# Performance work log

Hardware: AMD Instinct MI355X
Metric: run time of the kernel (lower is better)

The kernel has to match this reference:

```python
import jax, jax.numpy as jnp
import numpy as np
import math

B, S, H, N = 1, 4096, 1024, 16
HN = H // N  # 64

def setup_inputs() -> dict:
    key = jax.random.key(0)
    k1, k2, k3 = jax.random.split(key, 3)
    hidden_states = jax.random.normal(k1, (B, S, H), dtype=jnp.float32)
    # lower-triangular causal mask, float {0,1}, broadcastable to [b,np,s,s]
    ltor_mask = jnp.tril(jnp.ones((1, 1, S, S), dtype=jnp.float32))
    w_qkv = jax.random.normal(k2, (3 * H, H), dtype=jnp.float32) * 0.02
    b_qkv = jnp.zeros((3 * H,), dtype=jnp.float32)
    w_dense = jax.random.normal(k3, (H, H), dtype=jnp.float32) * 0.02
    b_dense = jnp.zeros((H,), dtype=jnp.float32)
    return {"hidden_states": hidden_states, "ltor_mask": ltor_mask,
            "w_qkv": w_qkv, "b_qkv": b_qkv,
            "w_dense": w_dense, "b_dense": b_dense}

def reference(hidden_states, ltor_mask, w_qkv, b_qkv, w_dense, b_dense):
    b, s, h = hidden_states.shape
    # fused QKV projection: [b,s,3h]
    mixed = jnp.einsum('bsh,oh->bso', hidden_states, w_qkv) + b_qkv
    q, k, v = jnp.split(mixed, 3, axis=-1)
    # [b,s,h] -> [b,n,s,hn]
    def heads(t):
        return t.reshape(b, s, N, HN).transpose(0, 2, 1, 3)
    q, k, v = heads(q), heads(k), heads(v)
    # raw scores [b,n,s,s]
    scores = jnp.einsum('bnqd,bnkd->bnqk', q, k) / math.sqrt(HN)
    # multiplicative mask plus -10000 additive for masked positions
    scores = scores * ltor_mask - 10000.0 * (1.0 - ltor_mask)
    probs = jax.nn.softmax(scores, axis=-1)
    # attention dropout prob = 0.0 -> identity
    ctx = jnp.einsum('bnqk,bnkd->bnqd', probs, v)
    ctx = ctx.transpose(0, 2, 1, 3).reshape(b, s, h)
    out = jnp.einsum('bsh,oh->bso', ctx, w_dense) + b_dense
    # output dropout prob = 0.0 -> identity
    return out
```

## Files before the change

kernel.cpp:

```cpp
#include <hip/hip_runtime.h>
#include <hip/hip_bf16.h>

static constexpr int SEQ  = 4096;
static constexpr int HID  = 1024;
static constexpr int NHEAD = 16;
static constexpr int HDIM  = 64;
static constexpr int H3   = 3072;

typedef __attribute__((ext_vector_type(8))) __bf16 bf16x8;
typedef __attribute__((ext_vector_type(4))) float  f32x4;

__device__ __forceinline__ float bf2f(unsigned short u) {
    union { unsigned int u; float f; } v; v.u = ((unsigned int)u) << 16; return v.f;
}
__device__ __forceinline__ unsigned short f2bf(float f) {
    union { float f; unsigned int u; } v; v.f = f;
    unsigned int r = v.u + 0x7fffu + ((v.u >> 16) & 1u);
    return (unsigned short)(r >> 16);
}
__device__ __forceinline__ void gl_lds16(const unsigned short* g, unsigned short* l) {
    __builtin_amdgcn_global_load_lds(
        (const __attribute__((address_space(1))) void*)g,
        (__attribute__((address_space(3))) void*)l, 16, 0, 0);
}

struct Conv5 { const float* src[5]; unsigned short* dst[5]; };

__global__ __launch_bounds__(256) void convert5(Conv5 c) {
    constexpr int cnt[5]  = {4194304, 3145728, 3072, 1048576, 1024};
    constexpr int boff[5] = {0, 2048, 3584, 3586, 4098};
    const int b = blockIdx.x;
    int t = 0, rel = b;
#pragma unroll
    for (int k = 1; k < 5; ++k) if (b >= boff[k]) { t = k; rel = b - boff[k]; }
    const int base = rel * 2048 + threadIdx.x * 8;
    if (base >= cnt[t]) return;
    const float* s = c.src[t] + base;
    const float4 a = ((const float4*)s)[0];
    const float4 b2 = ((const float4*)s)[1];
    union { unsigned short v[8]; uint4 q; } u;
    u.v[0] = f2bf(a.x); u.v[1] = f2bf(a.y); u.v[2] = f2bf(a.z); u.v[3] = f2bf(a.w);
    u.v[4] = f2bf(b2.x); u.v[5] = f2bf(b2.y); u.v[6] = f2bf(b2.z); u.v[7] = f2bf(b2.w);
    *(uint4*)(c.dst[t] + base) = u.q;
}

template <int BM, int BN, int BK, typename OutT, bool VFUSE>
__global__ __launch_bounds__(256) void gemm_bt(
    const unsigned short* __restrict__ A, const unsigned short* __restrict__ B,
    const unsigned short* __restrict__ bias, OutT* __restrict__ C,
    unsigned short* __restrict__ vt,
    int M, int N, int K)
{
    constexpr int MI  = BM / 32;
    constexpr int NI  = BN / 32;
    constexpr int KC  = BK / 32;
    constexpr int CB  = BK / 8;
    constexpr int LSH = (BK == 32) ? 2 : 3;
    constexpr int RPC = 64 >> LSH;

    const int tid  = threadIdx.x;
    const int wave = tid >> 6, lane = tid & 63;
    const int quad = lane >> 4, c16 = lane & 15;
    const int m0 = blockIdx.y * BM, n0 = blockIdx.x * BN;
    const int wr = wave >> 1, wc = wave & 1;

    __shared__ __align__(16) unsigned short sA[BM * BK];
    __shared__ __align__(16) unsigned short sB[BN * BK];

    f32x4 acc[MI][NI];
#pragma unroll
    for (int i = 0; i < MI; ++i)
#pragma unroll
        for (int j = 0; j < NI; ++j) acc[i][j] = {0.f, 0.f, 0.f, 0.f};

    const int sr = lane >> LSH;
    const int sc = ((lane & (CB - 1)) ^ (sr & (CB - 1))) * 8;

    for (int k0 = 0; k0 < K; k0 += BK) {
#pragma unroll
        for (int cc = 0; cc < BM / RPC / 4; ++cc) {
            const int rbase = cc * (4 * RPC) + wave * RPC;
            gl_lds16(A + (size_t)(m0 + rbase + sr) * K + k0 + sc, &sA[rbase * BK]);
        }
#pragma unroll
        for (int cc = 0; cc < BN / RPC / 4; ++cc) {
            const int rbase = cc * (4 * RPC) + wave * RPC;
            gl_lds16(B + (size_t)(n0 + rbase + sr) * K + k0 + sc, &sB[rbase * BK]);
        }
        __syncthreads();

#pragma unroll
        for (int kc = 0; kc < KC; ++kc) {
            bf16x8 af[MI], bfr[NI];
#pragma unroll
            for (int i = 0; i < MI; ++i) {
                const int ra = wr * (BM / 2) + i * 16 + c16;
                af[i] = *(const bf16x8*)&sA[ra * BK + (((kc * 4 + quad) ^ ra) & (CB - 1)) * 8];
            }
#pragma unroll
            for (int j = 0; j < NI; ++j) {
                const int rb = wc * (BN / 2) + j * 16 + c16;
                bfr[j] = *(const bf16x8*)&sB[rb * BK + (((kc * 4 + quad) ^ rb) & (CB - 1)) * 8];
            }
#pragma unroll
            for (int i = 0; i < MI; ++i)
#pragma unroll
                for (int j = 0; j < NI; ++j)
                    acc[i][j] = __builtin_amdgcn_mfma_f32_16x16x32_bf16(af[i], bfr[j], acc[i][j], 0, 0, 0);
        }
        __syncthreads();
    }

    if constexpr (VFUSE) {
        if (n0 >= 2048) {
#pragma unroll
            for (int j = 0; j < NI; ++j) {
                const int col = n0 + wc * (BN / 2) + j * 16 + c16;
                const float bv = bf2f(bias[col]);
                const int d  = col - 2048;
                unsigned short* vrow = vt + (size_t)d * SEQ;
#pragma unroll
                for (int i = 0; i < MI; ++i) {
                    const int base32 = m0 + wr * (BM / 2) + (i >> 1) * 32;
                    const int phys = base32 + 8 * quad + 4 * (i & 1);
                    union { unsigned short u[4]; uint2 q2; } w;
#pragma unroll
                    for (int r = 0; r < 4; ++r) w.u[r] = f2bf(acc[i][j][r] + bv);
                    *(uint2*)&vrow[phys] = w.q2;
                }
            }
            return;
        }
    }

#pragma unroll
    for (int j = 0; j < NI; ++j) {
        const int col = n0 + wc * (BN / 2) + j * 16 + c16;
        const float bv = bf2f(bias[col]);
#pragma unroll
        for (int i = 0; i < MI; ++i) {
#pragma unroll
            for (int r = 0; r < 4; ++r) {
                const int row = m0 + wr * (BM / 2) + i * 16 + quad * 4 + r;
                const float v = acc[i][j][r] + bv;
                if constexpr (sizeof(OutT) == 2) C[(size_t)row * N + col] = (OutT)f2bf(v);
                else                             C[(size_t)row * N + col] = (OutT)v;
            }
        }
    }
}

__global__ __launch_bounds__(256) void attn_causal(
    const unsigned short* __restrict__ qkv, const unsigned short* __restrict__ vt,
    unsigned short* __restrict__ ctx)
{
    const int bx = blockIdx.x;
    const int n  = bx & 15;
    const int p  = bx >> 4;
    const int tid  = threadIdx.x;
    const int wave = tid >> 6, lane = tid & 63;
    const int quad = lane >> 4, c16 = lane & 15;
    const int qg  = wave & 1;
    const int kvh = wave >> 1;

    __shared__ __align__(16) unsigned short smem[16384];
    unsigned short* smem_k = smem;
    unsigned short* smem_v = smem + 8192;

    const float QS = 0.125f * 1.44269504f;
    const int srow8 = lane >> 3;
    const int scol8 = ((lane & 7) ^ (lane >> 3)) * 8;
    const int srow4 = lane >> 4;

#pragma unroll 1
    for (int t = 0; t < 2; ++t) {
        const int z = t ? p : 63 - p;
        const int qrow0 = z * 64 + qg * 32;

        bf16x8 qf[2][2];
#pragma unroll
        for (int wq = 0; wq < 2; ++wq)
#pragma unroll
            for (int kc = 0; kc < 2; ++kc) {
                bf16x8 q = *(const bf16x8*)(qkv + (size_t)(qrow0 + wq * 16 + c16) * H3 + n * HDIM + kc * 32 + quad * 8);
#pragma unroll
                for (int j = 0; j < 8; ++j) q[j] = (__bf16)((float)q[j] * QS);
                qf[wq][kc] = q;
            }

        f32x4 o[2][4];
#pragma unroll
        for (int wq = 0; wq < 2; ++wq)
#pragma unroll
            for (int dt = 0; dt < 4; ++dt) o[wq][dt] = {0.f, 0.f, 0.f, 0.f};
        float l_i[2] = {0.f, 0.f};

        const int nkb = (z + 2) >> 1;
        for (int kb = 0; kb < nkb; ++kb) {
            const int kv0 = kb * 128;
#pragma unroll
            for (int cc = 0; cc < 4; ++cc) {
                const int rb = wave * 32 + cc * 8;
                gl_lds16(qkv + (size_t)(kv0 + rb + srow8) * H3 + HID + n * HDIM + scol8,
                         &smem_k[rb * 64]);
            }
#pragma unroll
            for (int cc = 0; cc < 4; ++cc) {
                const int rb = wave * 16 + cc * 4;
                const int sv = (((lane & 15) ^ ((cc * 4 + srow4) & 15))) * 8;
                gl_lds16(vt + (size_t)(n * HDIM + rb + srow4) * SEQ + kv0 + sv,
                         &smem_v[rb * 128]);
            }
            __syncthreads();

            const int kv0w = kv0 + kvh * 64;
            if (kv0w <= qrow0 + 31) {
                f32x4 s[2][4];
#pragma unroll
                for (int wq = 0; wq < 2; ++wq)
#pragma unroll
                    for (int mt = 0; mt < 4; ++mt) s[wq][mt] = {0.f, 0.f, 0.f, 0.f};
#pragma unroll
                for (int mt = 0; mt < 4; ++mt) {
                    const int krow = kvh * 64 + mt * 16 + c16;
                    const bf16x8 kf0 = *(const bf16x8*)&smem_k[krow * 64 + ((quad)     ^ (krow & 7)) * 8];
                    const bf16x8 kf1 = *(const bf16x8*)&smem_k[krow * 64 + ((4 + quad) ^ (krow & 7)) * 8];
#pragma unroll
                    for (int wq = 0; wq < 2; ++wq) {
                        s[wq][mt] = __builtin_amdgcn_mfma_f32_16x16x32_bf16(kf0, qf[wq][0], s[wq][mt], 0, 0, 0);
                        s[wq][mt] = __builtin_amdgcn_mfma_f32_16x16x32_bf16(kf1, qf[wq][1], s[wq][mt], 0, 0, 0);
                    }
                }

#pragma unroll
                for (int wq = 0; wq < 2; ++wq) {
                    if (kv0w + 63 > qrow0 + wq * 16) {
                        const int q_g = qrow0 + wq * 16 + c16;
#pragma unroll
                        for (int mt = 0; mt < 4; ++mt)
#pragma unroll
                            for (int r = 0; r < 4; ++r) {
                                const int kv = kv0w + mt * 16 + quad * 4 + r;
                                if (kv > q_g) s[wq][mt][r] = -30000.0f;
                            }
                    }
                    float rs = 0.f;
#pragma unroll
                    for (int mt = 0; mt < 4; ++mt)
#pragma unroll
                        for (int r = 0; r < 4; ++r) {
                            const float pp = __builtin_amdgcn_exp2f(s[wq][mt][r]);
                            s[wq][mt][r] = pp;
                            rs += pp;
                        }
                    l_i[wq] += rs;
                }

                bf16x8 pf[2][2];
#pragma unroll
                for (int wq = 0; wq < 2; ++wq)
#pragma unroll
                    for (int kc = 0; kc < 2; ++kc) {
                        union { __bf16 b[8]; bf16x8 v; } pp;
#pragma unroll
                        for (int r = 0; r < 4; ++r) {
                            pp.b[r]     = (__bf16)s[wq][2 * kc][r];
                            pp.b[4 + r] = (__bf16)s[wq][2 * kc + 1][r];
                        }
                        pf[wq][kc] = pp.v;
                    }

#pragma unroll
                for (int kc = 0; kc < 2; ++kc) {
#pragma unroll
                    for (int dt = 0; dt < 4; ++dt) {
                        const int vrow = dt * 16 + c16;
                        const int pc8 = (kvh * 8 + kc * 4 + quad) ^ (vrow & 15);
                        const bf16x8 vf = *(const bf16x8*)&smem_v[vrow * 128 + pc8 * 8];
#pragma unroll
                        for (int wq = 0; wq < 2; ++wq)
                            o[wq][dt] = __builtin_amdgcn_mfma_f32_16x16x32_bf16(vf, pf[wq][kc], o[wq][dt], 0, 0, 0);
                    }
                }
            }
            __syncthreads();
        }

#pragma unroll
        for (int wq = 0; wq < 2; ++wq) {
            l_i[wq] += __shfl_xor(l_i[wq], 16);
            l_i[wq] += __shfl_xor(l_i[wq], 32);
        }

        float* cb = (float*)smem;
        float* lb = (float*)(smem + 8704);
        unsigned short* fb = smem + 8832;

        if (kvh == 0) {
#pragma unroll
            for (int wq = 0; wq < 2; ++wq) {
#pragma unroll
                for (int dt = 0; dt < 4; ++dt)
                    *(f32x4*)&cb[(qg * 32 + wq * 16 + c16) * 68 + dt * 16 + quad * 4] = o[wq][dt];
                if (quad == 0) lb[qg * 32 + wq * 16 + c16] = l_i[wq];
            }
        }
        __syncthreads();
        if (kvh == 1) {
#pragma unroll
            for (int wq = 0; wq < 2; ++wq) {
                const float inv = 1.0f / (l_i[wq] + lb[qg * 32 + wq * 16 + c16]);
#pragma unroll
                for (int dt = 0; dt < 4; ++dt) {
                    const f32x4 pv = *(const f32x4*)&cb[(qg * 32 + wq * 16 + c16) * 68 + dt * 16 + quad * 4];
                    union { unsigned short u[4]; uint2 q2; } w;
#pragma unroll
                    for (int r = 0; r < 4; ++r) w.u[r] = f2bf((o[wq][dt][r] + pv[r]) * inv);
                    *(uint2*)&fb[(qg * 32 + wq * 16 + c16) * 72 + dt * 16 + quad * 4] = w.q2;
                }
            }
        }
        __syncthreads();

        const int qr = tid >> 2;
        const int xc = (tid & 3) * 16;
        unsigned short* dst = ctx + (size_t)(z * 64 + qr) * HID + n * HDIM + xc;
        *(uint4*)dst       = *(const uint4*)&fb[qr * 72 + xc];
        *(uint4*)(dst + 8) = *(const uint4*)&fb[qr * 72 + xc + 8];

        __syncthreads();
    }
}

extern "C" void kernel_launch(void* const* d_in, const int* in_sizes, int n_in,
                              void* d_out, int out_size, void* d_ws, size_t ws_size,
                              hipStream_t stream)
{
    unsigned short* base = (unsigned short*)d_ws;

    unsigned short* hs_c = base;
    unsigned short* wq_c = hs_c + 4194304;
    unsigned short* bq_c = wq_c + 3145728;
    unsigned short* wd_c = bq_c + 3072;
    unsigned short* bd_c = wd_c + 1048576;
    unsigned short* qkv  = bd_c + 1024;
    unsigned short* vt   = qkv + (size_t)SEQ * H3;
    unsigned short* ctx  = hs_c;

    Conv5 c;
    c.src[0] = (const float*)d_in[0]; c.src[1] = (const float*)d_in[2];
    c.src[2] = (const float*)d_in[3]; c.src[3] = (const float*)d_in[4];
    c.src[4] = (const float*)d_in[5];
    c.dst[0] = hs_c; c.dst[1] = wq_c; c.dst[2] = bq_c; c.dst[3] = wd_c; c.dst[4] = bd_c;
    hipLaunchKernelGGL(convert5, dim3(4099), dim3(256), 0, stream, c);

    hipLaunchKernelGGL((gemm_bt<128, 128, 32, unsigned short, true>),
                       dim3(H3 / 128, SEQ / 128), dim3(256), 0, stream,
                       hs_c, wq_c, bq_c, qkv, vt, SEQ, H3, HID);
    hipLaunchKernelGGL(attn_causal, dim3(NHEAD * (SEQ / 128)), dim3(256), 0, stream,
                       qkv, vt, ctx);
    hipLaunchKernelGGL((gemm_bt<64, 128, 64, float, false>),
                       dim3(HID / 128, SEQ / 64), dim3(256), 0, stream,
                       ctx, wd_c, bd_c, (float*)d_out, (unsigned short*)nullptr, SEQ, HID, HID);
}
```

Measured before the change: 248.0 us.

## Restructure causal attention to one 128-row Q tile per block with full KV per wave

Attention now gives each block a single 128-row query tile and processes tiles heaviest-first, instead of pairing two 64-row tiles per block. Each wave owns 32 query rows and processes the whole 128-key block, which removes the cross-wave split-KV reduction through LDS and its extra barriers. MFMA sections are wrapped in s_setprio hints. The QKV GEMM K-tile is also raised to 64. The trade-off is coarser load balancing across blocks, more score registers per wave, and more wasted masked work on diagonal blocks.

```diff
diff --git a/kernel.cpp b/kernel.cpp
--- a/kernel.cpp
+++ b/kernel.cpp
@@ -156,179 +156,147 @@
 {
     const int bx = blockIdx.x;
     const int n  = bx & 15;
-    const int p  = bx >> 4;
+    const int u  = bx >> 4;
+    const int t  = (u < 16) ? (31 - u) : (u - 16);
+
     const int tid  = threadIdx.x;
     const int wave = tid >> 6, lane = tid & 63;
     const int quad = lane >> 4, c16 = lane & 15;
-    const int qg  = wave & 1;
-    const int kvh = wave >> 1;
 
     __shared__ __align__(16) unsigned short smem[16384];
     unsigned short* smem_k = smem;
     unsigned short* smem_v = smem + 8192;
 
+    const int qw0 = t * 128 + wave * 32;
+
     const float QS = 0.125f * 1.44269504f;
+    bf16x8 qf[2][2];
+#pragma unroll
+    for (int wq = 0; wq < 2; ++wq)
+#pragma unroll
+        for (int kc = 0; kc < 2; ++kc) {
+            bf16x8 q = *(const bf16x8*)(qkv + (size_t)(qw0 + wq * 16 + c16) * H3 + n * HDIM + kc * 32 + quad * 8);
+#pragma unroll
+            for (int j = 0; j < 8; ++j) q[j] = (__bf16)((float)q[j] * QS);
+            qf[wq][kc] = q;
+        }
+
+    f32x4 o[2][4];
+#pragma unroll
+    for (int wq = 0; wq < 2; ++wq)
+#pragma unroll
+        for (int dt = 0; dt < 4; ++dt) o[wq][dt] = {0.f, 0.f, 0.f, 0.f};
+    float l_i[2] = {0.f, 0.f};
+
     const int srow8 = lane >> 3;
     const int scol8 = ((lane & 7) ^ (lane >> 3)) * 8;
     const int srow4 = lane >> 4;
 
-#pragma unroll 1
-    for (int t = 0; t < 2; ++t) {
-        const int z = t ? p : 63 - p;
-        const int qrow0 = z * 64 + qg * 32;
-
-        bf16x8 qf[2][2];
+    const int NK = t + 1;
+
+    for (int kb = 0; kb < NK; ++kb) {
+        const int kv0 = kb * 128;
+#pragma unroll
+        for (int cc = 0; cc < 4; ++cc) {
+            const int rb = wave * 32 + cc * 8;
+            gl_lds16(qkv + (size_t)(kv0 + rb + srow8) * H3 + HID + n * HDIM + scol8,
+                     &smem_k[rb * 64]);
+        }
+#pragma unroll
+        for (int cc = 0; cc < 4; ++cc) {
+            const int rb = wave * 16 + cc * 4;
+            const int sv = (((lane & 15) ^ ((cc * 4 + srow4) & 15))) * 8;
+            gl_lds16(vt + (size_t)(n * HDIM + rb + srow4) * SEQ + kv0 + sv,
+                     &smem_v[rb * 128]);
+        }
+        __syncthreads();
+
+        f32x4 s[2][8];
 #pragma unroll
         for (int wq = 0; wq < 2; ++wq)
 #pragma unroll
-            for (int kc = 0; kc < 2; ++kc) {
-                bf16x8 q = *(const bf16x8*)(qkv + (size_t)(qrow0 + wq * 16 + c16) * H3 + n * HDIM + kc * 32 + quad * 8);
-#pragma unroll
-                for (int j = 0; j < 8; ++j) q[j] = (__bf16)((float)q[j] * QS);
-                qf[wq][kc] = q;
-            }
-
-        f32x4 o[2][4];
-#pragma unroll
-        for (int wq = 0; wq < 2; ++wq)
-#pragma unroll
-            for (int dt = 0; dt < 4; ++dt) o[wq][dt] = {0.f, 0.f, 0.f, 0.f};
-        float l_i[2] = {0.f, 0.f};
-
-        const int nkb = (z + 2) >> 1;
-        for (int kb = 0; kb < nkb; ++kb) {
-            const int kv0 = kb * 128;
-#pragma unroll
-            for (int cc = 0; cc < 4; ++cc) {
-                const int rb = wave * 32 + cc * 8;
-                gl_lds16(qkv + (size_t)(kv0 + rb + srow8) * H3 + HID + n * HDIM + scol8,
-                         &smem_k[rb * 64]);
-            }
-#pragma unroll
-            for (int cc = 0; cc < 4; ++cc) {
-                const int rb = wave * 16 + cc * 4;
-                const int sv = (((lane & 15) ^ ((cc * 4 + srow4) & 15))) * 8;
-                gl_lds16(vt + (size_t)(n * HDIM + rb + srow4) * SEQ + kv0 + sv,
-                         &smem_v[rb * 128]);
-            }
-            __syncthreads();
-
-            const int kv0w = kv0 + kvh * 64;
-            if (kv0w <= qrow0 + 31) {
-                f32x4 s[2][4];
+            for (int mt = 0; mt < 8; ++mt) s[wq][mt] = {0.f, 0.f, 0.f, 0.f};
+        __builtin_amdgcn_s_setprio(1);
+#pragma unroll
+        for (int mt = 0; mt < 8; ++mt) {
+            const int krow = mt * 16 + c16;
+            const bf16x8 kf0 = *(const bf16x8*)&smem_k[krow * 64 + ((quad)     ^ (krow & 7)) * 8];
+            const bf16x8 kf1 = *(const bf16x8*)&smem_k[krow * 64 + ((4 + quad) ^ (krow & 7)) * 8];
+#pragma unroll
+            for (int wq = 0; wq < 2; ++wq) {
+                s[wq][mt] = __builtin_amdgcn_mfma_f32_16x16x32_bf16(kf0, qf[wq][0], s[wq][mt], 0, 0, 0);
+                s[wq][mt] = __builtin_amdgcn_mfma_f32_16x16x32_bf16(kf1, qf[wq][1], s[wq][mt], 0, 0, 0);
+            }
+        }
+        __builtin_amdgcn_s_setprio(0);
+
+#pragma unroll
+        for (int wq = 0; wq < 2; ++wq) {
+            if (kv0 + 127 > qw0 + wq * 16) {
+                const int q_g = qw0 + wq * 16 + c16;
+#pragma unroll
+                for (int mt = 0; mt < 8; ++mt)
+#pragma unroll
+                    for (int r = 0; r < 4; ++r) {
+                        const int kv = kv0 + mt * 16 + quad * 4 + r;
+                        if (kv > q_g) s[wq][mt][r] = -30000.0f;
+                    }
+            }
+            float rs = 0.f;
+#pragma unroll
+            for (int mt = 0; mt < 8; ++mt)
+#pragma unroll
+                for (int r = 0; r < 4; ++r) {
+                    const float pp = __builtin_amdgcn_exp2f(s[wq][mt][r]);
+                    s[wq][mt][r] = pp;
+                    rs += pp;
+                }
+            l_i[wq] += rs;
+        }
+
+        __builtin_amdgcn_s_setprio(1);
+#pragma unroll
+        for (int kcp = 0; kcp < 4; ++kcp) {
+            bf16x8 pf[2];
+#pragma unroll
+            for (int wq = 0; wq < 2; ++wq) {
+                union { __bf16 b[8]; bf16x8 v; } pp;
+#pragma unroll
+                for (int r = 0; r < 4; ++r) {
+                    pp.b[r]     = (__bf16)s[wq][2 * kcp][r];
+                    pp.b[4 + r] = (__bf16)s[wq][2 * kcp + 1][r];
+                }
+                pf[wq] = pp.v;
+            }
+#pragma unroll
+            for (int dt = 0; dt < 4; ++dt) {
+                const int vrow = dt * 16 + c16;
+                const int pc8 = (kcp * 4 + quad) ^ (vrow & 15);
+                const bf16x8 vf = *(const bf16x8*)&smem_v[vrow * 128 + pc8 * 8];
 #pragma unroll
                 for (int wq = 0; wq < 2; ++wq)
-#pragma unroll
-                    for (int mt = 0; mt < 4; ++mt) s[wq][mt] = {0.f, 0.f, 0.f, 0.f};
-#pragma unroll
-                for (int mt = 0; mt < 4; ++mt) {
-                    const int krow = kvh * 64 + mt * 16 + c16;
-                    const bf16x8 kf0 = *(const bf16x8*)&smem_k[krow * 64 + ((quad)     ^ (krow & 7)) * 8];
-                    const bf16x8 kf1 = *(const bf16x8*)&smem_k[krow * 64 + ((4 + quad) ^ (krow & 7)) * 8];
-#pragma unroll
-                    for (int wq = 0; wq < 2; ++wq) {
-                        s[wq][mt] = __builtin_amdgcn_mfma_f32_16x16x32_bf16(kf0, qf[wq][0], s[wq][mt], 0, 0, 0);
-                        s[wq][mt] = __builtin_amdgcn_mfma_f32_16x16x32_bf16(kf1, qf[wq][1], s[wq][mt], 0, 0, 0);
-                    }
-                }
-
-#pragma unroll
-                for (int wq = 0; wq < 2; ++wq) {
-                    if (kv0w + 63 > qrow0 + wq * 16) {
-                        const int q_g = qrow0 + wq * 16 + c16;
-#pragma unroll
-                        for (int mt = 0; mt < 4; ++mt)
-#pragma unroll
-                            for (int r = 0; r < 4; ++r) {
-                                const int kv = kv0w + mt * 16 + quad * 4 + r;
-                                if (kv > q_g) s[wq][mt][r] = -30000.0f;
-                            }
-                    }
-                    float rs = 0.f;
-#pragma unroll
-                    for (int mt = 0; mt < 4; ++mt)
-#pragma unroll
-                        for (int r = 0; r < 4; ++r) {
-                            const float pp = __builtin_amdgcn_exp2f(s[wq][mt][r]);
-                            s[wq][mt][r] = pp;
-                            rs += pp;
-                        }
-                    l_i[wq] += rs;
-                }
-
-                bf16x8 pf[2][2];
-#pragma unroll
-                for (int wq = 0; wq < 2; ++wq)
-#pragma unroll
-                    for (int kc = 0; kc < 2; ++kc) {
-                        union { __bf16 b[8]; bf16x8 v; } pp;
-#pragma unroll
-                        for (int r = 0; r < 4; ++r) {
-                            pp.b[r]     = (__bf16)s[wq][2 * kc][r];
-                            pp.b[4 + r] = (__bf16)s[wq][2 * kc + 1][r];
-                        }
-                        pf[wq][kc] = pp.v;
-                    }
-
-#pragma unroll
-                for (int kc = 0; kc < 2; ++kc) {
-#pragma unroll
-                    for (int dt = 0; dt < 4; ++dt) {
-                        const int vrow = dt * 16 + c16;
-                        const int pc8 = (kvh * 8 + kc * 4 + quad) ^ (vrow & 15);
-                        const bf16x8 vf = *(const bf16x8*)&smem_v[vrow * 128 + pc8 * 8];
-#pragma unroll
-                        for (int wq = 0; wq < 2; ++wq)
-                            o[wq][dt] = __builtin_amdgcn_mfma_f32_16x16x32_bf16(vf, pf[wq][kc], o[wq][dt], 0, 0, 0);
-                    }
-                }
-            }
-            __syncthreads();
-        }
-
-#pragma unroll
-        for (int wq = 0; wq < 2; ++wq) {
-            l_i[wq] += __shfl_xor(l_i[wq], 16);
-            l_i[wq] += __shfl_xor(l_i[wq], 32);
-        }
-
-        float* cb = (float*)smem;
-        float* lb = (float*)(smem + 8704);
-        unsigned short* fb = smem + 8832;
-
-        if (kvh == 0) {
-#pragma unroll
-            for (int wq = 0; wq < 2; ++wq) {
-#pragma unroll
-                for (int dt = 0; dt < 4; ++dt)
-                    *(f32x4*)&cb[(qg * 32 + wq * 16 + c16) * 68 + dt * 16 + quad * 4] = o[wq][dt];
-                if (quad == 0) lb[qg * 32 + wq * 16 + c16] = l_i[wq];
-            }
-        }
+                    o[wq][dt] = __builtin_amdgcn_mfma_f32_16x16x32_bf16(vf, pf[wq], o[wq][dt], 0, 0, 0);
+            }
+        }
+        __builtin_amdgcn_s_setprio(0);
+
         __syncthreads();
-        if (kvh == 1) {
-#pragma unroll
-            for (int wq = 0; wq < 2; ++wq) {
-                const float inv = 1.0f / (l_i[wq] + lb[qg * 32 + wq * 16 + c16]);
-#pragma unroll
-                for (int dt = 0; dt < 4; ++dt) {
-                    const f32x4 pv = *(const f32x4*)&cb[(qg * 32 + wq * 16 + c16) * 68 + dt * 16 + quad * 4];
-                    union { unsigned short u[4]; uint2 q2; } w;
-#pragma unroll
-                    for (int r = 0; r < 4; ++r) w.u[r] = f2bf((o[wq][dt][r] + pv[r]) * inv);
-                    *(uint2*)&fb[(qg * 32 + wq * 16 + c16) * 72 + dt * 16 + quad * 4] = w.q2;
-                }
-            }
-        }
-        __syncthreads();
-
-        const int qr = tid >> 2;
-        const int xc = (tid & 3) * 16;
-        unsigned short* dst = ctx + (size_t)(z * 64 + qr) * HID + n * HDIM + xc;
-        *(uint4*)dst       = *(const uint4*)&fb[qr * 72 + xc];
-        *(uint4*)(dst + 8) = *(const uint4*)&fb[qr * 72 + xc + 8];
-
-        __syncthreads();
+    }
+
+#pragma unroll
+    for (int wq = 0; wq < 2; ++wq) {
+        l_i[wq] += __shfl_xor(l_i[wq], 16);
+        l_i[wq] += __shfl_xor(l_i[wq], 32);
+        const float inv = 1.0f / l_i[wq];
+        const int q = qw0 + wq * 16 + c16;
+        unsigned short* dst = ctx + (size_t)q * HID + n * HDIM;
+#pragma unroll
+        for (int dt = 0; dt < 4; ++dt) {
+            union { unsigned short u[4]; uint2 q2; } w;
+#pragma unroll
+            for (int r = 0; r < 4; ++r) w.u[r] = f2bf(o[wq][dt][r] * inv);
+            *(uint2*)&dst[dt * 16 + quad * 4] = w.q2;
+        }
     }
 }
 
@@ -354,11 +322,13 @@
     c.dst[0] = hs_c; c.dst[1] = wq_c; c.dst[2] = bq_c; c.dst[3] = wd_c; c.dst[4] = bd_c;
     hipLaunchKernelGGL(convert5, dim3(4099), dim3(256), 0, stream, c);
 
-    hipLaunchKernelGGL((gemm_bt<128, 128, 32, unsigned short, true>),
+    hipLaunchKernelGGL((gemm_bt<128, 128, 64, unsigned short, true>),
                        dim3(H3 / 128, SEQ / 128), dim3(256), 0, stream,
                        hs_c, wq_c, bq_c, qkv, vt, SEQ, H3, HID);
-    hipLaunchKernelGGL(attn_causal, dim3(NHEAD * (SEQ / 128)), dim3(256), 0, stream,
+
+    hipLaunchKernelGGL(attn_causal, dim3(512), dim3(256), 0, stream,
                        qkv, vt, ctx);
+
     hipLaunchKernelGGL((gemm_bt<64, 128, 64, float, false>),
                        dim3(HID / 128, SEQ / 64), dim3(256), 0, stream,
                        ctx, wd_c, bd_c, (float*)d_out, (unsigned short*)nullptr, SEQ, HID, HID);
```

Result: no change. 252.1 us (+1.7%).
